# Performance work log

Hardware: AMD Instinct MI355X
Metric: run time of the kernel (lower is better)

Reference implementation:

```python
import jax, jax.numpy as jnp
import numpy as np

NUM_WIRES = 12
NUM_LAYERS = 4
BATCH = 16384


def setup_inputs() -> dict:
    key = jax.random.key(0)
    k1, k2, k3 = jax.random.split(key, 3)
    return {
        "inputs": jax.random.normal(k1, (BATCH, NUM_WIRES), jnp.float32),
        "params": jax.random.normal(k2, (NUM_LAYERS, NUM_WIRES), jnp.float32),
        "head_w": jax.random.normal(k3, (1, NUM_WIRES), jnp.float32) / np.sqrt(NUM_WIRES),
        "head_b": jnp.zeros((1,), jnp.float32),
    }


def _apply_1q_batched(state, gate, w):
    # state: (B, 2**n) complex; gate: (B, 2, 2) complex; wire w (0 = most significant, PennyLane convention)
    B = state.shape[0]
    s = state.reshape(B, 2 ** w, 2, -1)
    s = jnp.einsum('bij,bljr->blir', gate, s)
    return s.reshape(B, -1)


def _apply_1q_shared(state, gate, w):
    # gate: (2, 2) complex shared across batch
    B = state.shape[0]
    s = state.reshape(B, 2 ** w, 2, -1)
    s = jnp.einsum('ij,bljr->blir', gate, s)
    return s.reshape(B, -1)


def _apply_rz(state, theta, w):
    # diagonal gate: diag(e^{-i th/2}, e^{+i th/2})
    B = state.shape[0]
    ph = jnp.exp(1j * (theta * 0.5) * jnp.array([-1.0, 1.0], jnp.float32)).astype(jnp.complex64)
    s = state.reshape(B, 2 ** w, 2, -1) * ph.reshape(1, 1, 2, 1)
    return s.reshape(B, -1)


def _apply_cnot(state, c):
    # CNOT with control c, target c+1 (adjacent wires)
    B = state.shape[0]
    s = state.reshape(B, 2 ** c, 2, 2, -1)
    s = jnp.concatenate([s[:, :, 0:1], jnp.flip(s[:, :, 1:2], axis=3)], axis=2)
    return s.reshape(B, -1)


def _circuit(inputs, params):
    B, n = inputs.shape
    num_layers = params.shape[0]
    state = jnp.zeros((B, 2 ** n), jnp.complex64).at[:, 0].set(1.0)

    # RY(inputs[i]) encoding, per-sample angles
    half = inputs * 0.5
    cy, sy = jnp.cos(half), jnp.sin(half)  # (B, n)
    for i in range(n):
        ry = jnp.stack([jnp.stack([cy[:, i], -sy[:, i]], -1),
                        jnp.stack([sy[:, i],  cy[:, i]], -1)], -2).astype(jnp.complex64)  # (B,2,2)
        state = _apply_1q_batched(state, ry, i)

    for l in range(num_layers):
        for i in range(n):
            th = params[l, i] * 0.5
            ct, st = jnp.cos(th), jnp.sin(th)
            rx = jnp.stack([jnp.stack([ct + 0j, -1j * st]),
                            jnp.stack([-1j * st, ct + 0j])]).astype(jnp.complex64)  # (2,2)
            state = _apply_1q_shared(state, rx, i)
            state = _apply_rz(state, params[l, i], i)
        for i in range(n - 1):
            state = _apply_cnot(state, i)

    probs = jnp.abs(state) ** 2  # (B, 2**n) float32
    zvals = []
    for i in range(n):
        p = probs.reshape(B, 2 ** i, 2, -1)
        zvals.append(p[:, :, 0, :].sum((1, 2)) - p[:, :, 1, :].sum((1, 2)))
    return jnp.stack(zvals, -1)  # (B, n)


def reference(inputs, params, head_w, head_b):
    q_features = _circuit(inputs, params)            # (B, num_wires)
    out = q_features @ head_w.T + head_b             # (B, 1)
    return out.squeeze(-1)                           # (B,)
```

## Files before the change

### kernel.cpp

```cpp
#include <hip/hip_runtime.h>

#define NW 12

typedef float f2 __attribute__((ext_vector_type(2)));

__device__ constexpr int perm64c(int j) {
    j ^= (j >> 1) & 1;
    j ^= (j >> 1) & 2;
    j ^= (j >> 1) & 4;
    j ^= (j >> 1) & 8;
    j ^= (j >> 1) & 16;
    return j;
}

__device__ constexpr int ppar(int j, int k) {
    int p = 0;
    for (int i = 0; i <= k; ++i) p ^= (j >> (5 - i)) & 1;
    return p;
}

__device__ __forceinline__ f2 sp(float x) { f2 v; v.x = x; v.y = x; return v; }

__device__ __forceinline__ float elv(const f2* A, int j) {
    return (j & 1) ? A[j >> 1].y : A[j >> 1].x;
}

template<int PM>
__device__ __forceinline__ void rx_pk(f2* R, f2* I, f2 c, f2 s) {
    #pragma unroll
    for (int k0 = 0; k0 < 32; ++k0) {
        if (k0 & PM) continue;
        const int k1 = k0 | PM;
        const f2 ar = R[k0], ai = I[k0], br = R[k1], bi = I[k1];
        R[k0] = c * ar + s * bi;
        I[k0] = c * ai - s * br;
        R[k1] = c * br + s * ai;
        I[k1] = c * bi - s * ar;
    }
}

__device__ __forceinline__ void rx_pk0(f2* R, f2* I, f2 c, f2 s) {
    #pragma unroll
    for (int k = 0; k < 32; ++k) {
        const f2 Rs = R[k].yx, Is = I[k].yx;
        R[k] = c * R[k] + s * Is;
        I[k] = c * I[k] - s * Rs;
    }
}

__device__ __forceinline__ void rx_sweep(f2* R, f2* I, const float2* __restrict__ cs) {
    { const float2 q = cs[0]; rx_pk<16>(R, I, sp(q.x), sp(q.y)); }
    { const float2 q = cs[1]; rx_pk<8>(R, I, sp(q.x), sp(q.y)); }
    { const float2 q = cs[2]; rx_pk<4>(R, I, sp(q.x), sp(q.y)); }
    { const float2 q = cs[3]; rx_pk<2>(R, I, sp(q.x), sp(q.y)); }
    { const float2 q = cs[4]; rx_pk<1>(R, I, sp(q.x), sp(q.y)); }
    { const float2 q = cs[5]; rx_pk0(R, I, sp(q.x), sp(q.y)); }
}

__device__ __forceinline__ void diag_pk(f2* R, f2* I, const float4* __restrict__ z) {
    #pragma unroll
    for (int k = 0; k < 32; ++k) {
        const float4 q = z[k];
        f2 zx; zx.x = q.x; zx.y = q.y;
        f2 zy; zy.x = q.z; zy.y = q.w;
        const f2 nr = R[k] * zx - I[k] * zy;
        const f2 ni = I[k] * zx + R[k] * zy;
        R[k] = nr; I[k] = ni;
    }
}

__device__ __forceinline__ void perm_pk(f2* R, f2* I) {
    f2 tR[32], tI[32];
    #pragma unroll
    for (int k = 0; k < 32; ++k) {
        const int s0 = perm64c(2 * k);
        const int k2 = s0 >> 1;
        if (s0 & 1) { tR[k] = R[k2].yx; tI[k] = I[k2].yx; }
        else        { tR[k] = R[k2];    tI[k] = I[k2];    }
    }
    #pragma unroll
    for (int k = 0; k < 32; ++k) { R[k] = tR[k]; I[k] = tI[k]; }
}

__device__ __forceinline__ void cnot56_L2(f2* R, f2* I) {
    #pragma unroll
    for (int k = 0; k < 32; ++k) {
        R[k].y = __shfl_xor(R[k].y, 32, 64);
        I[k].y = __shfl_xor(I[k].y, 32, 64);
    }
}

__device__ __forceinline__ void cnot56_L1(f2* R, f2* I, int lane) {
    const bool c = (lane & 1) != 0;
    #pragma unroll
    for (int k = 0; k < 16; ++k) {
        const f2 a0 = R[k], a1 = R[k + 16], b0 = I[k], b1 = I[k + 16];
        R[k]      = c ? a1 : a0;  R[k + 16] = c ? a0 : a1;
        I[k]      = c ? b1 : b0;  I[k + 16] = c ? b0 : b1;
    }
}

template<bool PRE, bool POST>
__device__ __forceinline__ void tpose(float* pl, f2* R, f2* I, const int lane, const int rb) {
    char* base = reinterpret_cast<char*>(pl);
    const int ls = lane & 15;
    const int wb = lane << 8;
    #pragma unroll
    for (int g = 0; g < 16; ++g) {
        float4 v;
        v.x = elv(R, PRE ? perm64c(4 * g + 0) : 4 * g + 0);
        v.y = elv(R, PRE ? perm64c(4 * g + 1) : 4 * g + 1);
        v.z = elv(R, PRE ? perm64c(4 * g + 2) : 4 * g + 2);
        v.w = elv(R, PRE ? perm64c(4 * g + 3) : 4 * g + 3);
        *reinterpret_cast<float4*>(base + wb + ((g ^ ls) << 4)) = v;
    }
    #pragma unroll
    for (int k = 0; k < 32; ++k) {
        const int r0 = POST ? perm64c(2 * k) : 2 * k;
        const int r1 = r0 ^ 1;
        f2 nv;
        nv.x = *reinterpret_cast<const float*>(base + (rb ^ (((r0 & 15) << 4) | (r0 << 8))));
        nv.y = *reinterpret_cast<const float*>(base + (rb ^ (((r1 & 15) << 4) | (r1 << 8))));
        R[k] = nv;
    }
    #pragma unroll
    for (int g = 0; g < 16; ++g) {
        float4 v;
        v.x = elv(I, PRE ? perm64c(4 * g + 0) : 4 * g + 0);
        v.y = elv(I, PRE ? perm64c(4 * g + 1) : 4 * g + 1);
        v.z = elv(I, PRE ? perm64c(4 * g + 2) : 4 * g + 2);
        v.w = elv(I, PRE ? perm64c(4 * g + 3) : 4 * g + 3);
        *reinterpret_cast<float4*>(base + wb + ((g ^ ls) << 4)) = v;
    }
    #pragma unroll
    for (int k = 0; k < 32; ++k) {
        const int r0 = POST ? perm64c(2 * k) : 2 * k;
        const int r1 = r0 ^ 1;
        f2 nv;
        nv.x = *reinterpret_cast<const float*>(base + (rb ^ (((r0 & 15) << 4) | (r0 << 8))));
        nv.y = *reinterpret_cast<const float*>(base + (rb ^ (((r1 & 15) << 4) | (r1 << 8))));
        I[k] = nv;
    }
}

__global__ void qr_pre(const float* __restrict__ params,
                       float2* __restrict__ tabcs,
                       float* __restrict__ zpk)
{
    const int t = threadIdx.x;
    if (t < 48) {
        const int h = t / 6, k = t - h * 6;
        const int l = h >> 1;
        const int base = (((h & 3) == 0) || ((h & 3) == 3)) ? 6 : 0;
        const float th = 0.5f * params[l * 12 + base + k];
        tabcs[t] = make_float2(cosf(th), sinf(th));
    }
    if (t < 384) {
        const int h = t >> 6, j = t & 63;
        const int l = h >> 1;
        const int base = (((h & 3) == 0) || ((h & 3) == 3)) ? 6 : 0;
        float pr = 1.f, pi = 0.f;
        for (int k = 0; k < 6; ++k) {
            const float th = 0.5f * params[l * 12 + base + k];
            const float c = cosf(th), s = sinf(th);
            const float ss = (j & (32 >> k)) ? s : -s;
            const float nr = pr * c - pi * ss;
            pi = pr * ss + pi * c;
            pr = nr;
        }
        float* q = zpk + (h * 32 + (j >> 1)) * 4;
        q[j & 1] = pr;
        q[2 + (j & 1)] = pi;
    }
}

__global__ __launch_bounds__(64, 1) void qr_main(
    const float* __restrict__ inputs,
    const float2* __restrict__ tabcs,
    const float4* __restrict__ zpk,
    const float* __restrict__ head_w,
    const float* __restrict__ head_b,
    float* __restrict__ out)
{
    __shared__ __align__(16) float pl[4096];
    const int lane = threadIdx.x;
    const int b = blockIdx.x;

    float cy[12], sy[12];
    #pragma unroll
    for (int i = 0; i < 12; ++i) {
        __sincosf(0.5f * inputs[b * 12 + i], &sy[i], &cy[i]);
    }

    float F = 1.f;
    #pragma unroll
    for (int i = 0; i < 6; ++i) F *= (lane & (32 >> i)) ? sy[i] : cy[i];

    float hi[8];
    #pragma unroll
    for (int m = 0; m < 8; ++m)
        hi[m] = ((m & 4) ? sy[6] : cy[6]) * ((m & 2) ? sy[7] : cy[7]) * ((m & 1) ? sy[8] : cy[8]);
    f2 lop[4];
    #pragma unroll
    for (int m = 0; m < 4; ++m) {
        const float q = ((m & 2) ? sy[9] : cy[9]) * ((m & 1) ? sy[10] : cy[10]);
        lop[m].x = q * cy[11];
        lop[m].y = q * sy[11];
    }

    f2 R[32], I[32];
    #pragma unroll
    for (int k = 0; k < 32; ++k) {
        R[k] = sp(F * hi[k >> 2]) * lop[k & 3];
        I[k] = sp(0.f);
    }

    const int rb = (((lane >> 2) << 4) | ((lane & 3) << 2));

    #pragma unroll 1
    for (int h = 0; h < 8; ++h) {
        rx_sweep(R, I, tabcs + h * 6);
        if (h < 6) diag_pk(R, I, zpk + h * 32);

        if (h == 1 || h == 5) {
            perm_pk(R, I);
            cnot56_L2(R, I);
        } else if (h == 3) {
            cnot56_L1(R, I, lane);
            perm_pk(R, I);
        } else if (h == 0 || h == 4) {
            tpose<false, false>(pl, R, I, lane, rb);
        } else if (h == 2) {
            tpose<true, true>(pl, R, I, lane, rb);
        } else if (h == 6) {
            tpose<false, true>(pl, R, I, lane, rb);
        }
    }

    float w[12];
    #pragma unroll
    for (int i = 0; i < 12; ++i) w[i] = head_w[i];

    float C = 0.f; int par = 0;
    #pragma unroll
    for (int i = 0; i < 6; ++i) {
        par ^= (lane >> (5 - i)) & 1;
        C += par ? -w[i] : w[i];
    }
    const float sg = par ? -1.f : 1.f;

    float phi = 0.f;
    #pragma unroll
    for (int j = 0; j < 64; ++j) {
        const float re = elv(R, j), im = elv(I, j);
        const float p = re * re + im * im;
        float D = 0.f;
        #pragma unroll
        for (int k = 0; k < 6; ++k) {
            D += ppar(j, k) ? -w[6 + k] : w[6 + k];
        }
        phi += (C + sg * D) * p;
    }

    #pragma unroll
    for (int m = 32; m; m >>= 1) phi += __shfl_xor(phi, m, 64);
    if (lane == 0) out[b] = phi + head_b[0];
}

extern "C" void kernel_launch(void* const* d_in, const int* in_sizes, int n_in,
                              void* d_out, int out_size, void* d_ws, size_t ws_size,
                              hipStream_t stream) {
    const float* inputs = (const float*)d_in[0];
    const float* params = (const float*)d_in[1];
    const float* head_w = (const float*)d_in[2];
    const float* head_b = (const float*)d_in[3];
    float* out = (float*)d_out;

    float2* tabcs = (float2*)d_ws;
    float*  zpk   = (float*)d_ws + 96;

    const int batch = in_sizes[0] / NW;

    qr_pre<<<1, 384, 0, stream>>>(params, tabcs, zpk);
    qr_main<<<batch, 64, 0, stream>>>(inputs, tabcs, (const float4*)zpk, head_w, head_b, out);
}
```

Measured before the change: 463.1 us.

## Process two batch samples per wavefront to interleave independent state vectors

Result: slower. 833.2 us (+79.9%).

```diff
diff --git a/kernel.cpp b/kernel.cpp
--- a/kernel.cpp
+++ b/kernel.cpp
@@ -182,64 +182,16 @@
     const float* __restrict__ head_b,
     float* __restrict__ out)
 {
-    __shared__ __align__(16) float pl[4096];
+    __shared__ __align__(16) float pl[8192];
     const int lane = threadIdx.x;
-    const int b = blockIdx.x;
-
-    float cy[12], sy[12];
-    #pragma unroll
-    for (int i = 0; i < 12; ++i) {
-        __sincosf(0.5f * inputs[b * 12 + i], &sy[i], &cy[i]);
-    }
-
-    float F = 1.f;
-    #pragma unroll
-    for (int i = 0; i < 6; ++i) F *= (lane & (32 >> i)) ? sy[i] : cy[i];
-
-    float hi[8];
-    #pragma unroll
-    for (int m = 0; m < 8; ++m)
-        hi[m] = ((m & 4) ? sy[6] : cy[6]) * ((m & 2) ? sy[7] : cy[7]) * ((m & 1) ? sy[8] : cy[8]);
-    f2 lop[4];
-    #pragma unroll
-    for (int m = 0; m < 4; ++m) {
-        const float q = ((m & 2) ? sy[9] : cy[9]) * ((m & 1) ? sy[10] : cy[10]);
-        lop[m].x = q * cy[11];
-        lop[m].y = q * sy[11];
-    }
-
-    f2 R[32], I[32];
-    #pragma unroll
-    for (int k = 0; k < 32; ++k) {
-        R[k] = sp(F * hi[k >> 2]) * lop[k & 3];
-        I[k] = sp(0.f);
-    }
+    const int b0 = blockIdx.x * 2;
 
     const int rb = (((lane >> 2) << 4) | ((lane & 3) << 2));
 
-    #pragma unroll 1
-    for (int h = 0; h < 8; ++h) {
-        rx_sweep(R, I, tabcs + h * 6);
-        if (h < 6) diag_pk(R, I, zpk + h * 32);
-
-        if (h == 1 || h == 5) {
-            perm_pk(R, I);
-            cnot56_L2(R, I);
-        } else if (h == 3) {
-            cnot56_L1(R, I, lane);
-            perm_pk(R, I);
-        } else if (h == 0 || h == 4) {
-            tpose<false, false>(pl, R, I, lane, rb);
-        } else if (h == 2) {
-            tpose<true, true>(pl, R, I, lane, rb);
-        } else if (h == 6) {
-            tpose<false, true>(pl, R, I, lane, rb);
-        }
-    }
-
     float w[12];
     #pragma unroll
     for (int i = 0; i < 12; ++i) w[i] = head_w[i];
+    const float hb = head_b[0];
 
     float C = 0.f; int par = 0;
     #pragma unroll
@@ -249,22 +201,106 @@
     }
     const float sg = par ? -1.f : 1.f;
 
-    float phi = 0.f;
+    f2 Ra[32], Ia[32], Rb[32], Ib[32];
+    {
+        float cy[12], sy[12];
+        #pragma unroll
+        for (int i = 0; i < 12; ++i)
+            __sincosf(0.5f * inputs[b0 * 12 + i], &sy[i], &cy[i]);
+        float F = 1.f;
+        #pragma unroll
+        for (int i = 0; i < 6; ++i) F *= (lane & (32 >> i)) ? sy[i] : cy[i];
+        float hi[8];
+        #pragma unroll
+        for (int m = 0; m < 8; ++m)
+            hi[m] = ((m & 4) ? sy[6] : cy[6]) * ((m & 2) ? sy[7] : cy[7]) * ((m & 1) ? sy[8] : cy[8]);
+        f2 lop[4];
+        #pragma unroll
+        for (int m = 0; m < 4; ++m) {
+            const float q = ((m & 2) ? sy[9] : cy[9]) * ((m & 1) ? sy[10] : cy[10]);
+            lop[m].x = q * cy[11];
+            lop[m].y = q * sy[11];
+        }
+        #pragma unroll
+        for (int k = 0; k < 32; ++k) { Ra[k] = sp(F * hi[k >> 2]) * lop[k & 3]; Ia[k] = sp(0.f); }
+    }
+    {
+        float cy[12], sy[12];
+        #pragma unroll
+        for (int i = 0; i < 12; ++i)
+            __sincosf(0.5f * inputs[(b0 + 1) * 12 + i], &sy[i], &cy[i]);
+        float F = 1.f;
+        #pragma unroll
+        for (int i = 0; i < 6; ++i) F *= (lane & (32 >> i)) ? sy[i] : cy[i];
+        float hi[8];
+        #pragma unroll
+        for (int m = 0; m < 8; ++m)
+            hi[m] = ((m & 4) ? sy[6] : cy[6]) * ((m & 2) ? sy[7] : cy[7]) * ((m & 1) ? sy[8] : cy[8]);
+        f2 lop[4];
+        #pragma unroll
+        for (int m = 0; m < 4; ++m) {
+            const float q = ((m & 2) ? sy[9] : cy[9]) * ((m & 1) ? sy[10] : cy[10]);
+            lop[m].x = q * cy[11];
+            lop[m].y = q * sy[11];
+        }
+        #pragma unroll
+        for (int k = 0; k < 32; ++k) { Rb[k] = sp(F * hi[k >> 2]) * lop[k & 3]; Ib[k] = sp(0.f); }
+    }
+
+    #pragma unroll 1
+    for (int h = 0; h < 8; ++h) {
+        rx_sweep(Ra, Ia, tabcs + h * 6);
+        rx_sweep(Rb, Ib, tabcs + h * 6);
+        if (h < 6) {
+            diag_pk(Ra, Ia, zpk + h * 32);
+            diag_pk(Rb, Ib, zpk + h * 32);
+        }
+
+        if (h == 1 || h == 5) {
+            perm_pk(Ra, Ia); cnot56_L2(Ra, Ia);
+            perm_pk(Rb, Ib); cnot56_L2(Rb, Ib);
+        } else if (h == 3) {
+            cnot56_L1(Ra, Ia, lane); perm_pk(Ra, Ia);
+            cnot56_L1(Rb, Ib, lane); perm_pk(Rb, Ib);
+        } else if (h == 0 || h == 4) {
+            tpose<false, false>(pl, Ra, Ia, lane, rb);
+            tpose<false, false>(pl + 4096, Rb, Ib, lane, rb);
+        } else if (h == 2) {
+            tpose<true, true>(pl, Ra, Ia, lane, rb);
+            tpose<true, true>(pl + 4096, Rb, Ib, lane, rb);
+        } else if (h == 6) {
+            tpose<false, true>(pl, Ra, Ia, lane, rb);
+            tpose<false, true>(pl + 4096, Rb, Ib, lane, rb);
+        }
+    }
+
+    float phiA = 0.f, phiB = 0.f;
     #pragma unroll
     for (int j = 0; j < 64; ++j) {
-        const float re = elv(R, j), im = elv(I, j);
-        const float p = re * re + im * im;
         float D = 0.f;
         #pragma unroll
-        for (int k = 0; k < 6; ++k) {
+        for (int k = 0; k < 6; ++k)
             D += ppar(j, k) ? -w[6 + k] : w[6 + k];
-        }
-        phi += (C + sg * D) * p;
-    }
-
-    #pragma unroll
-    for (int m = 32; m; m >>= 1) phi += __shfl_xor(phi, m, 64);
-    if (lane == 0) out[b] = phi + head_b[0];
+        const float cj = C + sg * D;
+        {
+            const float re = elv(Ra, j), im = elv(Ia, j);
+            phiA += cj * (re * re + im * im);
+        }
+        {
+            const float re = elv(Rb, j), im = elv(Ib, j);
+            phiB += cj * (re * re + im * im);
+        }
+    }
+
+    #pragma unroll
+    for (int m = 32; m; m >>= 1) {
+        phiA += __shfl_xor(phiA, m, 64);
+        phiB += __shfl_xor(phiB, m, 64);
+    }
+    if (lane == 0) {
+        out[b0]     = phiA + hb;
+        out[b0 + 1] = phiB + hb;
+    }
 }
 
 extern "C" void kernel_launch(void* const* d_in, const int* in_sizes, int n_in,
@@ -282,5 +318,5 @@
     const int batch = in_sizes[0] / NW;
 
     qr_pre<<<1, 384, 0, stream>>>(params, tabcs, zpk);
-    qr_main<<<batch, 64, 0, stream>>>(inputs, tabcs, (const float4*)zpk, head_w, head_b, out);
-}
+    qr_main<<<batch / 2, 64, 0, stream>>>(inputs, tabcs, (const float4*)zpk, head_w, head_b, out);
+}
```
